# Kernel tuning notes

Hardware: AMD Instinct MI355X
Metric: run time of the kernel (lower is better)

## Reference

```python
import jax, jax.numpy as jnp
import numpy as np

ALPHA = 10.0
DELTA = 0.0005
N = 16777216  # array_length


def setup_inputs() -> dict:
    key = jax.random.key(0)
    k1, k2 = jax.random.split(key)
    # learned parameter: in the original module this is initialized to linspace(0,1,N);
    # we use uniform [0,1] so the piecewise-linear search path is non-degenerate.
    indices = jax.random.uniform(k1, (N,), dtype=jnp.float32)
    array = jax.random.normal(k2, (N,), dtype=jnp.float32)
    return {"indices": indices, "array": array}


def reference(indices, array):
    # clamp learned knot positions to [0, 1]
    clamped = jnp.clip(indices, 0.0, 1.0)
    # piecewise-linear function f with x-knots = clamped, y-values = array.
    # jnp.interp requires ascending knots, so sort (x, y) pairs by x.
    order = jnp.argsort(clamped)
    xs = clamped[order]
    ys = array[order]
    # vectorized version of the per-index loop:
    #   left_item = f(clamped[i-1] + delta), this_item = f(clamped[i] - delta)
    q_left = clamped[:-1] + DELTA   # [N-1]
    q_this = clamped[1:] - DELTA    # [N-1]
    f_left = jnp.interp(q_left, xs, ys)
    f_this = jnp.interp(q_this, xs, ys)
    gap = jnp.maximum(f_left - f_this, 0.0)
    return ALPHA * jnp.sum(gap)
```

## Files before the change

kernel.cpp:

```cpp
#include <hip/hip_runtime.h>
#include <stdint.h>

#define ALPHA_C 10.0f
#define DELTA_C 0.0005f

typedef unsigned long long u64;
typedef unsigned u32;
typedef unsigned short u16;

#define KB2   (1u << 22)
#define NREG  8192
#define FPR   512
#define NBK   4096
#define RPB   2
#define FPB   1024
#define CAPB  4800
#define ACHUNK 32768
#define WR    5
#define WMAXB ((2 * WR + 1) * FPR)
#define Q38MAX ((1ULL << 38) - 1)

#define OLDKB (1u << 22)
#define SCAN_BLOCKS 1024
#define SCAN_TPB 256
#define SCAN_PER_THREAD 16

__device__ __forceinline__ float clamp01(float x) {
    return fminf(fmaxf(x, 0.0f), 1.0f);
}
__device__ __forceinline__ u64 q38_of(float x) {
    double d = (double)clamp01(x) * 274877906944.0;
    u64 q = (u64)d;
    return q > Q38MAX ? Q38MAX : q;
}
__device__ __forceinline__ u16 f2bf(float f) {
    u32 b = __float_as_uint(f);
    return (u16)((b + 0x8000u) >> 16);
}
__device__ __forceinline__ float bf2f(u32 h) {
    return __uint_as_float(h << 16);
}


__global__ void __launch_bounds__(256) k_hist(const float* __restrict__ ind,
                                              u32* __restrict__ cnt8k, int n) {
    __shared__ u32 lh[NREG];
    for (int k = threadIdx.x; k < (int)NREG; k += 256) lh[k] = 0;
    __syncthreads();
    int stride = gridDim.x * blockDim.x;
    for (int i = blockIdx.x * blockDim.x + threadIdx.x; i < n; i += stride)
        atomicAdd(&lh[(u32)(q38_of(ind[i]) >> 25)], 1u);
    __syncthreads();
    for (int k = threadIdx.x; k < (int)NREG; k += 256) {
        u32 v = lh[k];
        if (v) atomicAdd(&cnt8k[k], v);
    }
}

__global__ void __launch_bounds__(1024) k_scan8k(u32* __restrict__ cnt8k) {
    __shared__ u32 lds[1024];
    int tid = threadIdx.x;
    int base = tid * 8;
    u32 v[8]; u32 tot = 0;
#pragma unroll
    for (int k = 0; k < 8; ++k) { v[k] = cnt8k[base + k]; tot += v[k]; }
    lds[tid] = tot;
    __syncthreads();
    u32 x = tot;
    for (int s = 1; s < 1024; s <<= 1) {
        u32 y = (tid >= s) ? lds[tid - s] : 0u;
        __syncthreads();
        x += y; lds[tid] = x;
        __syncthreads();
    }
    u32 run = x - tot;
#pragma unroll
    for (int k = 0; k < 8; ++k) { u32 c = v[k]; cnt8k[base + k] = run; run += c; }
}

__global__ void k_prep(const u32* __restrict__ cnt8k, u32* __restrict__ bcur) {
    int b = blockIdx.x * 256 + threadIdx.x;
    if (b < (int)NBK) bcur[b] = cnt8k[b * RPB];
}

__global__ void __launch_bounds__(256) k_bucket(const float* __restrict__ ind,
                                                const float* __restrict__ arr,
                                                u32* __restrict__ bcur,
                                                u64* __restrict__ rec,
                                                u16* __restrict__ recy, int n) {
    __shared__ u32 hist[NBK];
    __shared__ u32 base[NBK];
    int cbase = blockIdx.x * ACHUNK;
    for (u32 k = threadIdx.x; k < (u32)NBK; k += 256) hist[k] = 0;
    __syncthreads();
    for (int k = threadIdx.x; k < ACHUNK; k += 256) {
        int i = cbase + k;
        if (i >= n) break;
        u32 bk = (u32)(q38_of(ind[i]) >> 26);
        atomicAdd(&hist[bk], 1u);
    }
    __syncthreads();
    for (u32 k = threadIdx.x; k < (u32)NBK; k += 256) {
        u32 h = hist[k];
        base[k] = h ? atomicAdd(&bcur[k], h) : 0u;
    }
    __syncthreads();
    for (int k = threadIdx.x; k < ACHUNK; k += 256) {
        int i = cbase + k;
        if (i >= n) break;
        u64 q = q38_of(ind[i]);
        u32 bk = (u32)(q >> 26);
        u32 d = atomicAdd(&base[bk], 1u);
        rec[d] = (q << 24) | (u64)(u32)i;
        recy[d] = f2bf(arr[i]);
    }
}

__global__ void __launch_bounds__(256) k_group_fine(const u32* __restrict__ cnt8k,
                                                    const u16* __restrict__ recy,
                                                    u16* __restrict__ foff16,
                                                    u64* __restrict__ rec, int n) {
    __shared__ u64 s2[CAPB];
    __shared__ u16 sy[CAPB];
    __shared__ u32 sc[FPB];
    __shared__ u32 lad[256];
    int b = blockIdx.x;
    u32 S = cnt8k[b * RPB];
    u32 E = (b * RPB + RPB < (int)NREG) ? cnt8k[b * RPB + RPB] : (u32)n;
    u32 cnt = E - S; if (cnt > CAPB) cnt = CAPB;
    for (u32 f = threadIdx.x; f < (u32)FPB; f += 256) sc[f] = 0;
    __syncthreads();
    for (u32 j = threadIdx.x; j < cnt; j += 256) {
        u32 fb = (u32)(rec[S + j] >> 40) & (FPB - 1);
        atomicAdd(&sc[fb], 1u);
    }
    __syncthreads();
    u32 c0 = sc[threadIdx.x * 4 + 0], c1 = sc[threadIdx.x * 4 + 1];
    u32 c2 = sc[threadIdx.x * 4 + 2], c3 = sc[threadIdx.x * 4 + 3];
    u32 tsum = c0 + c1 + c2 + c3;
    lad[threadIdx.x] = tsum;
    __syncthreads();
    u32 x = tsum;
    for (int st = 1; st < 256; st <<= 1) {
        u32 y = (threadIdx.x >= (u32)st) ? lad[threadIdx.x - st] : 0u;
        __syncthreads();
        x += y; lad[threadIdx.x] = x;
        __syncthreads();
    }
    u32 ex = x - tsum;
    u32 e0 = ex, e1 = ex + c0, e2 = ex + c0 + c1, e3 = ex + c0 + c1 + c2;
    sc[threadIdx.x * 4 + 0] = e0; sc[threadIdx.x * 4 + 1] = e1;
    sc[threadIdx.x * 4 + 2] = e2; sc[threadIdx.x * 4 + 3] = e3;
    __syncthreads();
    {
        u32 fb0 = threadIdx.x * 4;
        u32 rs0 = sc[fb0 & ~511u];
        u32 gb  = (u32)b * FPB + fb0;
        foff16[gb + 0] = (u16)(e0 + c0 - rs0);
        foff16[gb + 1] = (u16)(e1 + c1 - rs0);
        foff16[gb + 2] = (u16)(e2 + c2 - rs0);
        foff16[gb + 3] = (u16)(e3 + c3 - rs0);
    }
    __syncthreads();
    for (u32 j = threadIdx.x; j < cnt; j += 256) {
        u64 v = rec[S + j];
        u32 fb = (u32)(v >> 40) & (FPB - 1);
        u32 p = atomicAdd(&sc[fb], 1u);
        s2[p] = v;
        sy[p] = recy[S + j];
    }
    __syncthreads();
    for (u32 f = threadIdx.x; f < (u32)FPB; f += 256) {
        u32 st = f ? sc[f - 1] : 0u;
        u32 en = sc[f];
        for (u32 a = st + 1; a < en; ++a) {
            u64 key = s2[a]; u16 ky = sy[a]; u32 m = a;
            while (m > st && s2[m - 1] > key) { s2[m] = s2[m - 1]; sy[m] = sy[m - 1]; --m; }
            s2[m] = key; sy[m] = ky;
        }
    }
    __syncthreads();
    for (u32 j = threadIdx.x; j < cnt; j += 256) {
        u64 v = s2[j];
        u32 i   = (u32)(v & 0xFFFFFFu);
        u32 xlo = (u32)(v >> 24) & 0xFFFFu;
        u32 ybf = (u32)sy[j];
        rec[S + j] = ((u64)xlo << 40) | ((u64)ybf << 24) | (u64)i;
    }
}

__device__ __forceinline__ float feval2(u64 qq, u32 baseB, u32 nw,
                                        const u32* pos,
                                        const u64* __restrict__ fdata, u32 n) {
    u32 wb = (u32)(qq >> 16) - baseB;
    u32 ql = (u32)(qq & 0xFFFFu);
    u32 bs = pos[wb], be = pos[wb + 1];
    u32 c = 0;
    for (u32 p = bs; p < be; ++p)
        c += ((u32)(fdata[p] >> 40) <= ql) ? 1u : 0u;
    u32 P = bs + c;
    if (P == 0)  return bf2f((u32)(fdata[0] >> 24) & 0xFFFFu);
    if (P >= n)  return bf2f((u32)(fdata[n - 1] >> 24) & 0xFFFFu);
    u64 dlo = fdata[P - 1];
    u64 dhi = fdata[P];
    u32 wl = wb; while (wl > 0 && pos[wl] > P - 1) --wl;
    u32 wh = wb; while (wh + 1 < nw && pos[wh + 1] <= P) ++wh;
    u64 loQ = (((u64)(baseB + wl)) << 16) | (dlo >> 40);
    u64 hiQ = (((u64)(baseB + wh)) << 16) | (dhi >> 40);
    float loY = bf2f((u32)(dlo >> 24) & 0xFFFFu);
    float hiY = bf2f((u32)(dhi >> 24) & 0xFFFFu);
    if (hiQ == loQ) return loY;
    float dq = (float)(qq - loQ);
    float dd = (float)(hiQ - loQ);
    return loY + (dq / dd) * (hiY - loY);
}

__global__ void __launch_bounds__(512) k_eval(const u32* __restrict__ cnt8k,
        const u16* __restrict__ foff16, const u64* __restrict__ fdata,
        u32* __restrict__ oval, int n) {
    __shared__ u32 pos[WMAXB + 1];
    int r = blockIdx.x;
    int r0 = r - WR; if (r0 < 0) r0 = 0;
    int r1 = r + WR; if (r1 > (int)NREG - 1) r1 = (int)NREG - 1;
    u32 nw = (u32)(r1 - r0 + 1) << 9;
    u32 baseB = (u32)r0 << 9;
    for (u32 k = threadIdx.x; k < nw; k += 512) {
        u32 reg = (u32)r0 + (k >> 9);
        pos[1 + k] = cnt8k[reg] + (u32)foff16[(reg << 9) + (k & 511u)];
    }
    if (threadIdx.x == 0) pos[0] = cnt8k[r0];
    __syncthreads();
    u32 s = cnt8k[r];
    u32 e = (r + 1 < (int)NREG) ? cnt8k[r + 1] : (u32)n;
    u32 selfoff = ((u32)(r - r0)) << 9;
    for (u32 t = s + threadIdx.x; t < e; t += 512) {
        u64 d = fdata[t];
        u32 lo = 0;
#pragma unroll
        for (u32 st = 256; st; st >>= 1)
            if (t >= pos[selfoff + lo + st]) lo += st;
        u64 xq = (((u64)((u32)r * FPR + lo)) << 16) | (d >> 40);
        u32 i = (u32)(d & 0xFFFFFFu);
        float x = (float)((double)xq * 3.63797880709171295e-12);
        float qpf = x + DELTA_C;
        float qmf = x - DELTA_C;
        u64 qp = q38_of(qpf);
        u64 qm = q38_of(qmf);
        float fp = feval2(qp, baseB, nw, pos, fdata, (u32)n);
        float fm = feval2(qm, baseB, nw, pos, fdata, (u32)n);
        u32 o = ((u32)f2bf(fp) << 16) | (u32)f2bf(fm);
        __builtin_nontemporal_store(o, &oval[i]);
    }
}

__global__ void __launch_bounds__(256) k_pair2(const u32* __restrict__ oval,
                                               float* __restrict__ out, int n) {
    int stride = gridDim.x * blockDim.x;
    float sum = 0.0f;
    for (int j = blockIdx.x * blockDim.x + threadIdx.x; j < n - 1; j += stride) {
        u32 a = oval[j], b = oval[j + 1];
        sum += fmaxf(bf2f(a >> 16) - bf2f(b & 0xFFFFu), 0.0f);
    }
    float w = sum;
    for (int s = 32; s > 0; s >>= 1) w += __shfl_down(w, s, 64);
    __shared__ float wsum[4];
    if ((threadIdx.x & 63) == 0) wsum[threadIdx.x >> 6] = w;
    __syncthreads();
    if (threadIdx.x == 0)
        atomicAdd(out, ALPHA_C * (wsum[0] + wsum[1] + wsum[2] + wsum[3]));
}


__device__ __forceinline__ int bucket_of(float x) {
    int b = (int)(x * (float)OLDKB);
    b = b < 0 ? 0 : b;
    b = b > (int)OLDKB - 1 ? (int)OLDKB - 1 : b;
    return b;
}

__global__ void scan1(u32* __restrict__ off, u32* __restrict__ bsums) {
    __shared__ u32 lds[SCAN_TPB];
    int base = blockIdx.x * (SCAN_TPB * SCAN_PER_THREAD) + threadIdx.x * SCAN_PER_THREAD;
    u32 v[SCAN_PER_THREAD];
    u32 tot = 0;
#pragma unroll
    for (int k = 0; k < SCAN_PER_THREAD; ++k) { v[k] = off[base + k]; tot += v[k]; }
    lds[threadIdx.x] = tot;
    __syncthreads();
    u32 x = tot;
    for (int s = 1; s < SCAN_TPB; s <<= 1) {
        u32 y = (threadIdx.x >= (u32)s) ? lds[threadIdx.x - s] : 0u;
        __syncthreads();
        x += y; lds[threadIdx.x] = x;
        __syncthreads();
    }
    if (threadIdx.x == SCAN_TPB - 1) bsums[blockIdx.x] = x;
    u32 run = x - tot;
#pragma unroll
    for (int k = 0; k < SCAN_PER_THREAD; ++k) { u32 c = v[k]; off[base + k] = run; run += c; }
}

__global__ void scan2(u32* __restrict__ bsums) {
    __shared__ u32 lds[SCAN_BLOCKS];
    int tid = threadIdx.x;
    u32 v = bsums[tid];
    lds[tid] = v;
    __syncthreads();
    u32 x = v;
    for (int s = 1; s < SCAN_BLOCKS; s <<= 1) {
        u32 y = (tid >= s) ? lds[tid - s] : 0u;
        __syncthreads();
        x += y; lds[tid] = x;
        __syncthreads();
    }
    bsums[tid] = x - v;
}

__global__ void scan3(u32* __restrict__ off, const u32* __restrict__ bsums) {
    int base = blockIdx.x * (SCAN_TPB * SCAN_PER_THREAD);
    u32 add = bsums[blockIdx.x];
#pragma unroll
    for (int k = 0; k < SCAN_PER_THREAD; ++k)
        off[base + k * SCAN_TPB + threadIdx.x] += add;
}

__global__ void hist_kernel(const float* __restrict__ ind, u32* __restrict__ off, int n) {
    int i = blockIdx.x * blockDim.x + threadIdx.x;
    if (i < n) atomicAdd(&off[bucket_of(clamp01(ind[i]))], 1u);
}

__global__ void scatter_kernel(const float* __restrict__ ind, const float* __restrict__ arr,
                               u32* __restrict__ off, float2* __restrict__ buck, int n) {
    int i = blockIdx.x * blockDim.x + threadIdx.x;
    if (i < n) {
        float x = clamp01(ind[i]);
        u32 p = atomicAdd(&off[bucket_of(x)], 1u);
        buck[p] = make_float2(x, arr[i]);
    }
}

__device__ float feval(float q, const u32* __restrict__ off, const float2* __restrict__ buck) {
    int b = bucket_of(q);
    u32 s = (b == 0) ? 0u : off[b - 1];
    u32 e = off[b];
    float loX = -1e30f, loY = 0.0f, hiX = 1e30f, hiY = 0.0f;
    for (u32 u = s; u < e; ++u) {
        float2 p = buck[u];
        if (p.x <= q) { if (p.x >= loX) { loX = p.x; loY = p.y; } }
        else          { if (p.x <  hiX) { hiX = p.x; hiY = p.y; } }
    }
    if (loX == -1e30f) {
        int bl = b;
        while (bl > 0) {
            --bl;
            u32 s2 = (bl == 0) ? 0u : off[bl - 1];
            u32 e2 = off[bl];
            if (e2 > s2) {
                for (u32 u = s2; u < e2; ++u) {
                    float2 p = buck[u];
                    if (p.x >= loX) { loX = p.x; loY = p.y; }
                }
                break;
            }
        }
    }
    if (hiX == 1e30f) {
        int br = b;
        while (br < (int)OLDKB - 1) {
            ++br;
            u32 s2 = off[br - 1];
            u32 e2 = off[br];
            if (e2 > s2) {
                for (u32 u = s2; u < e2; ++u) {
                    float2 p = buck[u];
                    if (p.x < hiX) { hiX = p.x; hiY = p.y; }
                }
                break;
            }
        }
    }
    if (loX == -1e30f) return hiY;
    if (hiX ==  1e30f) return loY;
    return loY + (q - loX) * (hiY - loY) / (hiX - loX);
}

__global__ void query_kernel(const float* __restrict__ ind, const u32* __restrict__ off,
                             const float2* __restrict__ buck, float* __restrict__ out, int nterm) {
    int j = blockIdx.x * blockDim.x + threadIdx.x;
    float term = 0.0f;
    if (j < nterm) {
        float c0 = clamp01(ind[j]);
        float c1 = clamp01(ind[j + 1]);
        float fa = feval(c0 + DELTA_C, off, buck);
        float fb = feval(c1 - DELTA_C, off, buck);
        term = fmaxf(fa - fb, 0.0f);
    }
    float w = term;
    for (int s = 32; s > 0; s >>= 1) w += __shfl_down(w, s, 64);
    __shared__ float wsum[4];
    if ((threadIdx.x & 63) == 0) wsum[threadIdx.x >> 6] = w;
    __syncthreads();
    if (threadIdx.x == 0) atomicAdd(out, ALPHA_C * (wsum[0] + wsum[1] + wsum[2] + wsum[3]));
}


extern "C" void kernel_launch(void* const* d_in, const int* in_sizes, int n_in,
                              void* d_out, int out_size, void* d_ws, size_t ws_size,
                              hipStream_t stream) {
    const float* ind = (const float*)d_in[0];
    const float* arr = (const float*)d_in[1];
    float* out = (float*)d_out;
    int n = in_sizes[0];

    const int tpb = 256;
    int nblk = (n + tpb - 1) / tpb;
    uint8_t* w = (uint8_t*)d_ws;

    const size_t FOFF_SZ = (size_t)KB2 * 2;
    const size_t AUX = (size_t)1 << 20;
    size_t SZ8 = (size_t)n * 8, SZ4 = (size_t)n * 4;
    size_t base = FOFF_SZ + AUX;
    size_t need = base + SZ8 + SZ4;

    if (n <= (1 << 24) && ws_size >= need) {
        u16* foff16 = (u16*)w;
        u32* cnt8k  = (u32*)(w + FOFF_SZ);
        u32* bcur   = (u32*)(w + FOFF_SZ + 32768);
        u64* rec    = (u64*)(w + base);
        u16* recy   = (u16*)(w + base + SZ8);
        u32* oval   = (u32*)(w + base + SZ8);

        hipMemsetAsync(cnt8k, 0, NREG * 4, stream);
        hipMemsetAsync(out, 0, sizeof(float) * (size_t)out_size, stream);

        int abks = (n + ACHUNK - 1) / ACHUNK;
        k_hist<<<512, 256, 0, stream>>>(ind, cnt8k, n);
        k_scan8k<<<1, 1024, 0, stream>>>(cnt8k);
        k_prep<<<(NBK + 255) / 256, 256, 0, stream>>>(cnt8k, bcur);
        k_bucket<<<abks, 256, 0, stream>>>(ind, arr, bcur, rec, recy, n);
        k_group_fine<<<NBK, 256, 0, stream>>>(cnt8k, recy, foff16, rec, n);
        k_eval<<<NREG, 512, 0, stream>>>(cnt8k, foff16, rec, oval, n);
        k_pair2<<<2048, 256, 0, stream>>>(oval, out, n);
    } else {
        const size_t FO = (size_t)OLDKB * 4;
        u32* off = (u32*)w;
        u32* bsums = (u32*)(w + FO);
        float2* buck = (float2*)(w + FO + 4096);

        hipMemsetAsync(off, 0, FO, stream);
        hipMemsetAsync(out, 0, sizeof(float) * (size_t)out_size, stream);

        hist_kernel<<<nblk, tpb, 0, stream>>>(ind, off, n);
        scan1<<<SCAN_BLOCKS, SCAN_TPB, 0, stream>>>(off, bsums);
        scan2<<<1, SCAN_BLOCKS, 0, stream>>>(bsums);
        scan3<<<SCAN_BLOCKS, SCAN_TPB, 0, stream>>>(off, bsums);
        scatter_kernel<<<nblk, tpb, 0, stream>>>(ind, arr, off, buck, n);
        int nterm = n - 1;
        query_kernel<<<(nterm + tpb - 1) / tpb, tpb, 0, stream>>>(ind, off, buck, out, nterm);
    }
}
```

Before: 1.869 ms.

## Replace per-query bucket scan with per-thread contiguous merge-walk evaluation

Each thread in k_eval now takes a contiguous run of sorted points instead of striding by 512, and evaluates both shifted queries with a monotone merge pointer that advances through the sorted knot data. This replaces the per-query linear count over a fine bucket and the backward/forward window searches. The goal is to cut redundant global loads and scanning work. In exchange, consecutive threads now read non-adjacent addresses, so loads are less coalesced, and per-thread work becomes serial and depends on how many knots the queries skip over.

```diff
diff --git a/kernel.cpp b/kernel.cpp
--- a/kernel.cpp
+++ b/kernel.cpp
@@ -189,32 +189,6 @@
     }
 }
 
-__device__ __forceinline__ float feval2(u64 qq, u32 baseB, u32 nw,
-                                        const u32* pos,
-                                        const u64* __restrict__ fdata, u32 n) {
-    u32 wb = (u32)(qq >> 16) - baseB;
-    u32 ql = (u32)(qq & 0xFFFFu);
-    u32 bs = pos[wb], be = pos[wb + 1];
-    u32 c = 0;
-    for (u32 p = bs; p < be; ++p)
-        c += ((u32)(fdata[p] >> 40) <= ql) ? 1u : 0u;
-    u32 P = bs + c;
-    if (P == 0)  return bf2f((u32)(fdata[0] >> 24) & 0xFFFFu);
-    if (P >= n)  return bf2f((u32)(fdata[n - 1] >> 24) & 0xFFFFu);
-    u64 dlo = fdata[P - 1];
-    u64 dhi = fdata[P];
-    u32 wl = wb; while (wl > 0 && pos[wl] > P - 1) --wl;
-    u32 wh = wb; while (wh + 1 < nw && pos[wh + 1] <= P) ++wh;
-    u64 loQ = (((u64)(baseB + wl)) << 16) | (dlo >> 40);
-    u64 hiQ = (((u64)(baseB + wh)) << 16) | (dhi >> 40);
-    float loY = bf2f((u32)(dlo >> 24) & 0xFFFFu);
-    float hiY = bf2f((u32)(dhi >> 24) & 0xFFFFu);
-    if (hiQ == loQ) return loY;
-    float dq = (float)(qq - loQ);
-    float dd = (float)(hiQ - loQ);
-    return loY + (dq / dd) * (hiY - loY);
-}
-
 __global__ void __launch_bounds__(512) k_eval(const u32* __restrict__ cnt8k,
         const u16* __restrict__ foff16, const u64* __restrict__ fdata,
         u32* __restrict__ oval, int n) {
@@ -232,22 +206,74 @@
     __syncthreads();
     u32 s = cnt8k[r];
     u32 e = (r + 1 < (int)NREG) ? cnt8k[r + 1] : (u32)n;
+    u32 cnt = e - s;
+    if (cnt == 0) return;
     u32 selfoff = ((u32)(r - r0)) << 9;
-    for (u32 t = s + threadIdx.x; t < e; t += 512) {
+    u32 wend = pos[nw];
+    u32 G = (cnt + 511) >> 9;
+    u32 t0 = s + threadIdx.x * G;
+    if (t0 >= e) return;
+    u32 t1 = t0 + G; if (t1 > e) t1 = e;
+
+    u32 kb = 0;
+#pragma unroll
+    for (u32 st = 256; st; st >>= 1)
+        if (pos[selfoff + kb + st] <= t0) kb += st;
+
+    u32 Pp = 0, wbp = 0, lowbp = 0; u64 lop = 0;
+    u32 Pm = 0, wbm = 0, lowbm = 0; u64 lom = 0;
+    bool inited = false;
+
+    auto mstep = [&](u64 qq, u32& P, u32& wb, u64& lo, u32& lowb) -> float {
+        u64 hi = 0; bool hasHi = false;
+        while (P < wend) {
+            u64 dd = fdata[P];
+            u64 key = (((u64)(baseB + wb)) << 16) | (dd >> 40);
+            if (key > qq) { hi = dd; hasHi = true; break; }
+            lo = dd; lowb = wb; ++P;
+            while (wb + 1 < nw && P >= pos[wb + 1]) ++wb;
+        }
+        if (!hasHi) return (P > 0) ? bf2f((u32)(lo >> 24) & 0xFFFFu) : 0.0f;
+        float hiY = bf2f((u32)(hi >> 24) & 0xFFFFu);
+        if (P == 0) return hiY;
+        float loY = bf2f((u32)(lo >> 24) & 0xFFFFu);
+        u64 loQ = (((u64)(baseB + lowb)) << 16) | (lo >> 40);
+        u64 hiQ = (((u64)(baseB + wb)) << 16) | (hi >> 40);
+        if (hiQ == loQ) return loY;
+        float dq = (float)(qq - loQ);
+        float dd2 = (float)(hiQ - loQ);
+        return loY + (dq / dd2) * (hiY - loY);
+    };
+
+    for (u32 t = t0; t < t1; ++t) {
+        while (pos[selfoff + kb + 1] <= t) ++kb;
         u64 d = fdata[t];
-        u32 lo = 0;
-#pragma unroll
-        for (u32 st = 256; st; st >>= 1)
-            if (t >= pos[selfoff + lo + st]) lo += st;
-        u64 xq = (((u64)((u32)r * FPR + lo)) << 16) | (d >> 40);
+        u64 xq = (((u64)((u32)r * FPR + kb)) << 16) | (d >> 40);
         u32 i = (u32)(d & 0xFFFFFFu);
         float x = (float)((double)xq * 3.63797880709171295e-12);
         float qpf = x + DELTA_C;
         float qmf = x - DELTA_C;
         u64 qp = q38_of(qpf);
         u64 qm = q38_of(qmf);
-        float fp = feval2(qp, baseB, nw, pos, fdata, (u32)n);
-        float fm = feval2(qm, baseB, nw, pos, fdata, (u32)n);
+        if (!inited) {
+            inited = true;
+            wbp = (u32)(qp >> 16) - baseB;
+            Pp = pos[wbp]; lowbp = wbp;
+            if (Pp > 0) {
+                while (lowbp > 0 && pos[lowbp] > Pp - 1) --lowbp;
+                lop = fdata[Pp - 1];
+            }
+            while (wbp + 1 < nw && Pp >= pos[wbp + 1]) ++wbp;
+            wbm = (u32)(qm >> 16) - baseB;
+            Pm = pos[wbm]; lowbm = wbm;
+            if (Pm > 0) {
+                while (lowbm > 0 && pos[lowbm] > Pm - 1) --lowbm;
+                lom = fdata[Pm - 1];
+            }
+            while (wbm + 1 < nw && Pm >= pos[wbm + 1]) ++wbm;
+        }
+        float fp = mstep(qp, Pp, wbp, lop, lowbp);
+        float fm = mstep(qm, Pm, wbm, lom, lowbm);
         u32 o = ((u32)f2bf(fp) << 16) | (u32)f2bf(fm);
         __builtin_nontemporal_store(o, &oval[i]);
     }
```

After: 1.904 ms. About the same (+1.8%).
